# Optimization experiments

Measured on AMD Instinct MI355X. Metric: run time of the kernel, lower is better.

The kernel has to match this reference:

```python
import jax, jax.numpy as jnp
import numpy as np

N_EMBD = 256; N_HEAD = 16; CTX = 2048
V_HD = 32; KV_RANK = 32; Q_RANK = 96
ROPE_HD = 64; NOPE_HD = 32; HEAD_D = ROPE_HD + NOPE_HD  # 96
N_KEEP = CTX // 4  # 512
C_CURV = 1.0
EPS = 1e-6
B, T = 2, 2048


def rmsnorm(x, w):
    return x * jax.lax.rsqrt(jnp.mean(x * x, axis=-1, keepdims=True) + EPS) * w


def logmap(x, u, c):
    # log map from hyperbolic point x toward u (Poincare ball, curvature c)
    xn = jnp.linalg.norm(x, axis=-1, keepdims=True)
    sf = 2.0 / (1.0 + c * xn ** 2)                      # scaling_factor(x, c)
    mx = -x
    un = jnp.linalg.norm(u, axis=-1, keepdims=True)
    ip = jnp.sum(mx * u, axis=-1, keepdims=True)
    num = (1 + 2 * c * ip + c * un ** 2) * mx + (1 - c * xn ** 2) * u
    den = 1 + 2 * c * ip + (c ** 2) * (xn ** 2) * (un ** 2)
    mob = num / den                                      # mobius_addition(-x, u, c)
    an = jnp.linalg.norm(mob, axis=-1, keepdims=True)
    cf = 2.0 / (sf * (c ** 0.5))
    arg = jnp.clip(jnp.sqrt(c) * jnp.sqrt(an), -0.999, 0.999)
    return cf * jnp.arctanh(arg) * (mob / an)


def rope_apply(x, cos_seq, sin_seq):
    # x: [B,H,T,D]; cos/sin: [T,D//2] -> broadcast [1,1,T,D//2]
    c = cos_seq[None, None]; s = sin_seq[None, None]
    xr, xi = jnp.split(x, 2, axis=-1)
    return jnp.concatenate([xr * c - xi * s, xr * s + xi * c], axis=-1)


def attn(q, k, v, causal):
    d = q.shape[-1]
    s = jnp.einsum('bhqd,bhkd->bhqk', q, k) / jnp.sqrt(jnp.asarray(d, q.dtype))
    if causal:
        mask = jnp.tril(jnp.ones((s.shape[-2], s.shape[-1]), bool))
        s = jnp.where(mask, s, -jnp.inf)
    p = jax.nn.softmax(s, axis=-1)
    return jnp.einsum('bhqk,bhkd->bhqd', p, v)


def setup_inputs() -> dict:
    key = jax.random.key(0)
    ks = jax.random.split(key, 20)
    w = lambda k, shp: (jax.random.normal(k, shp, jnp.float32) * 0.02)
    NOPE_DIM = N_HEAD * NOPE_HD   # 512
    ROPE_DIM = N_HEAD * ROPE_HD   # 1024
    VAL_DIM = N_HEAD * V_HD       # 512
    # precompute_freqs_cis(rope_head_dim, ctx_len)
    freqs = 1.0 / (10000.0 ** (np.arange(0, ROPE_HD, 2, dtype=np.float32) / ROPE_HD))
    t = np.arange(CTX, dtype=np.float32)
    ang = np.outer(t, freqs)
    return {
        'x': jax.random.normal(ks[0], (B, T, N_EMBD), jnp.float32),
        'W_cq': w(ks[1], (N_EMBD, Q_RANK)),
        'q_norm_w': jnp.ones((Q_RANK,), jnp.float32),
        'W_dqn': w(ks[2], (Q_RANK, NOPE_DIM)),
        'W_dqr': w(ks[3], (Q_RANK, ROPE_DIM)),
        'W_ckv': w(ks[4], (N_EMBD, KV_RANK)),
        'kv_norm_w': jnp.ones((KV_RANK,), jnp.float32),
        'W_dkn': w(ks[5], (KV_RANK, NOPE_DIM)),
        'W_dv': w(ks[6], (KV_RANK, VAL_DIM)),
        'W_kr': w(ks[7], (N_EMBD, ROPE_HD)),
        'W_imp': w(ks[8], (N_EMBD, 1)),
        'b_imp': jnp.zeros((1,), jnp.float32),
        'W_selk': w(ks[9], (N_EMBD, N_HEAD * HEAD_D)),
        'W_selv': w(ks[10], (N_EMBD, VAL_DIM)),
        'W_wink': w(ks[11], (N_EMBD, N_HEAD * HEAD_D)),
        'W_winv': w(ks[12], (N_EMBD, VAL_DIM)),
        'W_gate': w(ks[13], (N_EMBD, 3)),
        'b_gate': jnp.zeros((3,), jnp.float32),
        'W_proj': w(ks[14], (N_HEAD * V_HD, N_EMBD)),
        'cos_f': jnp.asarray(np.cos(ang)),
        'sin_f': jnp.asarray(np.sin(ang)),
    }


def reference(x, W_cq, q_norm_w, W_dqn, W_dqr, W_ckv, kv_norm_w, W_dkn, W_dv, W_kr,
              W_imp, b_imp, W_selk, W_selv, W_wink, W_winv, W_gate, b_gate, W_proj,
              cos_f, sin_f):
    Bx, Tx, C = x.shape
    ref = jnp.pad(x[:, :-1, :], ((0, 0), (1, 0), (0, 0)))   # calculate_reference_point
    xh = logmap(ref, x, C_CURV)
    # compressed query path
    nq = rmsnorm(xh @ W_cq, q_norm_w)
    qn = (nq @ W_dqn).reshape(Bx, Tx, N_HEAD, NOPE_HD).transpose(0, 2, 1, 3)
    qr = (nq @ W_dqr).reshape(Bx, Tx, N_HEAD, ROPE_HD).transpose(0, 2, 1, 3)
    qr = rope_apply(qr, cos_f[:Tx], sin_f[:Tx])
    q = jnp.concatenate([qn, qr], axis=-1)                  # [B,H,T,96]
    # branch gate
    bw = jax.nn.softmax(jnp.mean(x @ W_gate + b_gate, axis=1), axis=-1)  # [B,3]
    # compressed KV path
    nkv = rmsnorm(x @ W_ckv, kv_norm_w)
    kn = (nkv @ W_dkn).reshape(Bx, Tx, N_HEAD, NOPE_HD).transpose(0, 2, 1, 3)
    v = (nkv @ W_dv).reshape(Bx, Tx, N_HEAD, V_HD).transpose(0, 2, 1, 3)
    kr = rope_apply((x @ W_kr)[:, None], cos_f[:Tx], sin_f[:Tx])  # [B,1,T,64]
    kr = jnp.broadcast_to(kr, (Bx, N_HEAD, Tx, ROPE_HD))
    k = jnp.concatenate([kn, kr], axis=-1)
    out_cmp = attn(q, k, v, causal=True)
    # token-selection branch (top-k important tokens, sorted)
    scores = (x @ W_imp + b_imp)[..., 0]                    # [B,T]
    _, idx = jax.lax.top_k(scores, min(N_KEEP, Tx))
    idx = jnp.sort(idx, axis=1)
    sel = jnp.take_along_axis(x, idx[:, :, None], axis=1)   # [B,K,C]
    sk = (sel @ W_selk).reshape(Bx, -1, N_HEAD, HEAD_D).transpose(0, 2, 1, 3)
    sv = (sel @ W_selv).reshape(Bx, -1, N_HEAD, V_HD).transpose(0, 2, 1, 3)
    out_sel = attn(q, sk, sv, causal=False)
    # sliding-window branch (training path -> full sequence, causal)
    wk = (x @ W_wink).reshape(Bx, Tx, N_HEAD, HEAD_D).transpose(0, 2, 1, 3)
    wv = (x @ W_winv).reshape(Bx, Tx, N_HEAD, V_HD).transpose(0, 2, 1, 3)
    out_win = attn(q, wk, wv, causal=True)
    w3 = bw[:, :, None, None, None]
    out = w3[:, 0] * out_cmp + w3[:, 1] * out_sel + w3[:, 2] * out_win
    out = out.transpose(0, 2, 1, 3).reshape(Bx, Tx, N_HEAD * V_HD)
    return out @ W_proj
```

## Files before the change

### kernel.cpp

```cpp
#include <hip/hip_runtime.h>
#include <hip/hip_bf16.h>
#include <math.h>

#define TT 2048
#define NE 256
#define NHEAD 16

typedef __attribute__((ext_vector_type(8))) short bf16x8;
typedef __attribute__((ext_vector_type(4))) float f32x4;
typedef __attribute__((ext_vector_type(16))) float f32x16;
typedef unsigned short ushort;
typedef __attribute__((ext_vector_type(8))) unsigned short us8;

__device__ __forceinline__ short f2bf(float x) {
  __hip_bfloat16 h = __float2bfloat16(x);
  return *reinterpret_cast<short*>(&h);
}
__device__ __forceinline__ float bf2f(ushort u) {
  unsigned v = ((unsigned)u) << 16;
  return __uint_as_float(v);
}

__global__ __launch_bounds__(256) void prep_kernel(
    const float* __restrict__ x, ushort* __restrict__ xhb, ushort* __restrict__ xbf,
    const float* __restrict__ W_dqn, const float* __restrict__ W_dqr,
    const float* __restrict__ W_dkn, const float* __restrict__ W_dv,
    const float* __restrict__ W_selk, const float* __restrict__ W_selv,
    const float* __restrict__ W_wink, const float* __restrict__ W_winv,
    const float* __restrict__ W_proj, const float* __restrict__ W_cq,
    const float* __restrict__ W_ckv, const float* __restrict__ W_kr,
    const float* __restrict__ W_gate, const float* __restrict__ W_imp,
    ushort* __restrict__ Wt_q, ushort* __restrict__ Wt_kv,
    ushort* __restrict__ Wt_sel, ushort* __restrict__ Wt_win,
    ushort* __restrict__ Wt_proj, ushort* __restrict__ Wt_cq,
    ushort* __restrict__ Wt_nkv, float* __restrict__ gacc) {
  __shared__ float red[16];
  int bx = blockIdx.x, tid = threadIdx.x;
  if (bx < 4096) {
    int row = bx;
    int t = row & (TT - 1);
    float uv = x[row * NE + tid];
    float rv = (t == 0) ? 0.f : x[row * NE - NE + tid];
    xbf[row * NE + tid] = (ushort)f2bf(uv);
    float a = rv * rv, bq = uv * uv, c2 = -rv * uv;
#pragma unroll
    for (int off = 32; off > 0; off >>= 1) {
      a += __shfl_down(a, off, 64);
      bq += __shfl_down(bq, off, 64);
      c2 += __shfl_down(c2, off, 64);
    }
    if ((tid & 63) == 0) {
      int w = tid >> 6;
      red[w] = a; red[4 + w] = bq; red[8 + w] = c2;
    }
    __syncthreads();
    float xn2 = red[0] + red[1] + red[2] + red[3];
    float un2 = red[4] + red[5] + red[6] + red[7];
    float ip  = red[8] + red[9] + red[10] + red[11];
    float den = 1.f + 2.f * ip + xn2 * un2;
    float mob = ((1.f + 2.f * ip + un2) * (-rv) + (1.f - xn2) * uv) / den;
    float m2 = mob * mob;
#pragma unroll
    for (int off = 32; off > 0; off >>= 1) m2 += __shfl_down(m2, off, 64);
    if ((tid & 63) == 0) red[12 + (tid >> 6)] = m2;
    __syncthreads();
    float an2 = red[12] + red[13] + red[14] + red[15];
    float an = sqrtf(an2);
    float cf = 1.f + xn2;
    float arg = fminf(sqrtf(an), 0.999f);
    xhb[row * NE + tid] = (ushort)f2bf(cf * atanhf(arg) * mob / an);
    return;
  }
  int i = (bx - 4096) * 256 + tid;
  const float scale = 0.147244458176154f;
  if (i < 147456) {
    int k = i / 1536, n = i - k * 1536;
    float v = (n < 512) ? W_dqn[(size_t)k * 512 + n] : W_dqr[(size_t)k * 1024 + (n - 512)];
    Wt_q[(size_t)n * 96 + k] = (ushort)f2bf(v * scale);
  } else if (i < 180224) {
    int j = i - 147456;
    int k = j >> 10, n = j & 1023;
    float v = (n < 512) ? W_dkn[(size_t)k * 512 + n] : W_dv[(size_t)k * 512 + (n - 512)];
    Wt_kv[(size_t)n * 32 + k] = (ushort)f2bf(v);
  } else if (i < 704512) {
    int j = i - 180224;
    int k = j >> 11, n = j & 2047;
    float v = (n < 1536) ? W_selk[(size_t)k * 1536 + n] : W_selv[(size_t)k * 512 + (n - 1536)];
    Wt_sel[(size_t)n * 256 + k] = (ushort)f2bf(v);
  } else if (i < 1228800) {
    int j = i - 704512;
    int k = j >> 11, n = j & 2047;
    float v = (n < 1536) ? W_wink[(size_t)k * 1536 + n] : W_winv[(size_t)k * 512 + (n - 1536)];
    Wt_win[(size_t)n * 256 + k] = (ushort)f2bf(v);
  } else if (i < 1359872) {
    int j = i - 1228800;
    int k = j >> 8, n = j & 255;
    Wt_proj[(size_t)n * 512 + k] = (ushort)f2bf(W_proj[(size_t)k * 256 + n]);
  } else if (i < 1392640) {
    int j = i - 1359872;
    int k = j >> 7, n = j & 127;
    float v = (n < 96) ? W_cq[(size_t)k * 96 + n] : 0.f;
    Wt_cq[(size_t)n * 256 + k] = (ushort)f2bf(v);
  } else if (i < 1425408) {
    int j = i - 1392640;
    int k = j >> 7, n = j & 127;
    float v;
    if (n < 32) v = W_ckv[(size_t)k * 32 + n];
    else if (n < 96) v = W_kr[(size_t)k * 64 + (n - 32)];
    else if (n < 99) v = W_gate[(size_t)k * 3 + (n - 96)];
    else if (n == 99) v = W_imp[k];
    else v = 0.f;
    Wt_nkv[(size_t)n * 256 + k] = (ushort)f2bf(v);
  } else if (i < 1425414) {
    gacc[i - 1425408] = 0.f;
  }
}

__global__ __launch_bounds__(256) void gemm_kernel(const ushort* __restrict__ A,
                                                   const ushort* __restrict__ Bt,
                                                   void* __restrict__ Out,
                                                   const ushort* __restrict__ A2,
                                                   const ushort* __restrict__ Bt2,
                                                   void* __restrict__ Out2,
                                                   const int* __restrict__ selidx2,
                                                   const float* __restrict__ cosp,
                                                   const float* __restrict__ sinp,
                                                   float* __restrict__ gateacc,
                                                   const float* __restrict__ kvnw,
                                                   const float* __restrict__ qnw,
                                                   const float* __restrict__ bimp,
                                                   ushort* __restrict__ krbf_o,
                                                   float* __restrict__ scores_o,
                                                   int fusenorm,
                                                   int K, int ldo, int obf16, int ropemode,
                                                   int K2, int ldo2, int obf2, int rope2,
                                                   int xlim2, int ylim2) {
  __shared__ __align__(16) short gsm[2 * 128 * 40];
  short* As = gsm;
  short* Bs = gsm + 128 * 40;
  const int* selidx = nullptr;
  if (blockIdx.z == 1) {
    if ((int)blockIdx.x >= xlim2 || (int)blockIdx.y >= ylim2) return;
    A = A2; Bt = Bt2; Out = Out2; selidx = selidx2;
    K = K2; ldo = ldo2; obf16 = obf2; ropemode = rope2;
  }
  int m0 = blockIdx.x * 128, n0 = blockIdx.y * 128;
  int tid = threadIdx.x;
  int wv = tid >> 6, lane = tid & 63;
  int l15 = lane & 15, quad = lane >> 4;
  int wm = wv >> 1, wn = wv & 1;

  int r = tid >> 1, seg = tid & 1;
  int arow = m0 + r;
  if (selidx) arow = ((arow >> 9) * TT) + selidx[m0 + r];
  const ushort* ga = A + (size_t)arow * K + seg * 16;
  const ushort* gb = Bt + (size_t)(n0 + r) * K + seg * 16;

  f32x4 acc[4][4];
#pragma unroll
  for (int i = 0; i < 4; ++i)
#pragma unroll
    for (int j = 0; j < 4; ++j) acc[i][j] = (f32x4){0.f, 0.f, 0.f, 0.f};

  int nk = K >> 5;
  us8 apre0 = *(const us8*)ga, apre1 = *(const us8*)(ga + 8);
  us8 bpre0 = *(const us8*)gb, bpre1 = *(const us8*)(gb + 8);
  for (int kk = 0; kk < nk; ++kk) {
    __syncthreads();
    *(us8*)(As + r * 40 + seg * 16) = apre0;
    *(us8*)(As + r * 40 + seg * 16 + 8) = apre1;
    *(us8*)(Bs + r * 40 + seg * 16) = bpre0;
    *(us8*)(Bs + r * 40 + seg * 16 + 8) = bpre1;
    __syncthreads();
    if (kk + 1 < nk) {
      apre0 = *(const us8*)(ga + (kk + 1) * 32);
      apre1 = *(const us8*)(ga + (kk + 1) * 32 + 8);
      bpre0 = *(const us8*)(gb + (kk + 1) * 32);
      bpre1 = *(const us8*)(gb + (kk + 1) * 32 + 8);
    }
    bf16x8 af[4], bf[4];
#pragma unroll
    for (int mf = 0; mf < 4; ++mf)
      af[mf] = *(const bf16x8*)(As + (wm * 64 + mf * 16 + l15) * 40 + quad * 8);
#pragma unroll
    for (int nf = 0; nf < 4; ++nf)
      bf[nf] = *(const bf16x8*)(Bs + (wn * 64 + nf * 16 + l15) * 40 + quad * 8);
#pragma unroll
    for (int mf = 0; mf < 4; ++mf)
#pragma unroll
      for (int nf = 0; nf < 4; ++nf)
        acc[mf][nf] = __builtin_amdgcn_mfma_f32_16x16x32_bf16(af[mf], bf[nf], acc[mf][nf], 0, 0, 0);
  }

  if (fusenorm) {
    __syncthreads();
    float* sc = (float*)gsm;
    if (blockIdx.z == 0) {
      float ss[4][4];
#pragma unroll
      for (int mf = 0; mf < 4; ++mf)
#pragma unroll
        for (int reg = 0; reg < 4; ++reg) {
          float p = acc[mf][0][reg] * acc[mf][0][reg] + acc[mf][1][reg] * acc[mf][1][reg];
          if (wn == 0) p += acc[mf][2][reg] * acc[mf][2][reg] + acc[mf][3][reg] * acc[mf][3][reg];
#pragma unroll
          for (int off = 8; off > 0; off >>= 1) p += __shfl_xor(p, off, 64);
          ss[mf][reg] = p;
        }
      if (l15 == 0) {
#pragma unroll
        for (int mf = 0; mf < 4; ++mf)
#pragma unroll
          for (int reg = 0; reg < 4; ++reg)
            sc[wn * 128 + wm * 64 + mf * 16 + quad * 4 + reg] = ss[mf][reg];
      }
      __syncthreads();
#pragma unroll
      for (int mf = 0; mf < 4; ++mf) {
#pragma unroll
        for (int nf = 0; nf < 4; ++nf) {
          if (wn == 1 && nf >= 2) continue;
          int col = wn * 64 + nf * 16 + l15;
#pragma unroll
          for (int reg = 0; reg < 4; ++reg) {
            int rl = wm * 64 + mf * 16 + quad * 4 + reg;
            float sstot = sc[rl] + sc[128 + rl];
            float sca = rsqrtf(sstot / 96.f + 1e-6f) * qnw[col];
            ((ushort*)Out)[(size_t)(m0 + rl) * 96 + col] = (ushort)f2bf(acc[mf][nf][reg] * sca);
          }
        }
      }
    } else {
      if (wn == 1 && l15 < 3) {
        float g = 0.f;
#pragma unroll
        for (int mf = 0; mf < 4; ++mf)
#pragma unroll
          for (int reg = 0; reg < 4; ++reg) g += acc[mf][2][reg];
        atomicAdd(&gateacc[(m0 >> 11) * 3 + l15], g);
      }
      if (wn == 1 && l15 == 3) {
#pragma unroll
        for (int mf = 0; mf < 4; ++mf)
#pragma unroll
          for (int reg = 0; reg < 4; ++reg)
            scores_o[m0 + wm * 64 + mf * 16 + quad * 4 + reg] = acc[mf][2][reg] + bimp[0];
      }
      if (wn == 0) {
#pragma unroll
        for (int mf = 0; mf < 4; ++mf) {
          float ssr[4];
#pragma unroll
          for (int reg = 0; reg < 4; ++reg) {
            float p = acc[mf][0][reg] * acc[mf][0][reg] + acc[mf][1][reg] * acc[mf][1][reg];
#pragma unroll
            for (int off = 8; off > 0; off >>= 1) p += __shfl_xor(p, off, 64);
            ssr[reg] = p;
          }
#pragma unroll
          for (int nf = 0; nf < 2; ++nf) {
            int col = nf * 16 + l15;
#pragma unroll
            for (int reg = 0; reg < 4; ++reg) {
              int rl = wm * 64 + mf * 16 + quad * 4 + reg;
              float sca = rsqrtf(ssr[reg] / 32.f + 1e-6f) * kvnw[col];
              ((ushort*)Out)[(size_t)(m0 + rl) * 32 + col] = (ushort)f2bf(acc[mf][nf][reg] * sca);
            }
          }
        }
      }
      if (wn == 1) {
#pragma unroll
        for (int mf = 0; mf < 4; ++mf)
#pragma unroll
          for (int nf = 0; nf < 2; ++nf) {
            int dd = nf * 16 + l15;
#pragma unroll
            for (int reg = 0; reg < 4; ++reg) {
              int rl = wm * 64 + mf * 16 + quad * 4 + reg;
              sc[rl * 33 + dd] = acc[mf][nf][reg];
            }
          }
      }
      __syncthreads();
      if (wn == 0) {
#pragma unroll
        for (int mf = 0; mf < 4; ++mf)
#pragma unroll
          for (int nf = 2; nf < 4; ++nf) {
            int dd = (nf - 2) * 16 + l15;
#pragma unroll
            for (int reg = 0; reg < 4; ++reg) {
              int rl = wm * 64 + mf * 16 + quad * 4 + reg;
              int grow = m0 + rl;
              int t = grow & (TT - 1);
              float c = cosp[t * 32 + dd], s = sinp[t * 32 + dd];
              float xr = acc[mf][nf][reg], xi = sc[rl * 33 + dd];
              krbf_o[(size_t)grow * 64 + dd] = (ushort)f2bf(xr * c - xi * s);
              krbf_o[(size_t)grow * 64 + dd + 32] = (ushort)f2bf(xr * s + xi * c);
            }
          }
      }
    }
    return;
  }

  if (ropemode && blockIdx.y >= 4) {
#pragma unroll
    for (int mf = 0; mf < 4; ++mf) {
#pragma unroll
      for (int nf = 0; nf < 2; ++nf) {
        int dd = nf * 16 + l15;
#pragma unroll
        for (int reg = 0; reg < 4; ++reg) {
          int row = m0 + wm * 64 + mf * 16 + quad * 4 + reg;
          int t = row & (TT - 1);
          float c = cosp[t * 32 + dd], s = sinp[t * 32 + dd];
          float xr = acc[mf][nf][reg], xi = acc[mf][nf + 2][reg];
          int col = n0 + wn * 64 + nf * 16 + l15;
          size_t oi = (size_t)row * ldo + col;
          ((ushort*)Out)[oi] = (ushort)f2bf(xr * c - xi * s);
          ((ushort*)Out)[oi + 32] = (ushort)f2bf(xr * s + xi * c);
        }
      }
    }
    return;
  }
#pragma unroll
  for (int mf = 0; mf < 4; ++mf) {
#pragma unroll
    for (int nf = 0; nf < 4; ++nf) {
#pragma unroll
      for (int reg = 0; reg < 4; ++reg) {
        int row = m0 + wm * 64 + mf * 16 + quad * 4 + reg;
        int col = n0 + wn * 64 + nf * 16 + l15;
        size_t oi = (size_t)row * ldo + col;
        float v = acc[mf][nf][reg];
        if (obf16) ((ushort*)Out)[oi] = (ushort)f2bf(v);
        else ((float*)Out)[oi] = v;
      }
    }
  }
}

__global__ __launch_bounds__(1024) void topk_rank_kernel(const float* __restrict__ scores,
                                                         int* __restrict__ flags) {
  int b = blockIdx.y, blk = blockIdx.x;
  int tid = threadIdx.x;
  __shared__ unsigned sk[TT];
#pragma unroll
  for (int e = 0; e < 2; ++e) {
    int i = tid + e * 1024;
    float s = scores[b * TT + i];
    unsigned u = __float_as_uint(s);
    u = (u & 0x80000000u) ? ~u : (u | 0x80000000u);
    sk[i] = u;
  }
  __syncthreads();
  int e = blk * 64 + (tid >> 4);
  int sub = tid & 15;
  unsigned u = sk[e];
  int r = 0;
  int j0 = sub * 128;
#pragma unroll 8
  for (int j = j0; j < j0 + 128; ++j) {
    unsigned v = sk[j];
    r += (int)((v > u) || (v == u && j < e));
  }
#pragma unroll
  for (int off = 8; off > 0; off >>= 1) r += __shfl_down(r, off, 16);
  if (sub == 0) flags[b * TT + e] = (r < 512) ? 1 : 0;
}

__global__ __launch_bounds__(1024) void topk_scan_kernel(const int* __restrict__ flags,
                                                         int* __restrict__ selidx) {
  int b = blockIdx.x, tid = threadIdx.x;
  __shared__ int wsum[16];
  int2 f = *(const int2*)(flags + b * TT + 2 * tid);
  int local = f.x + f.y;
  int lane = tid & 63, wv = tid >> 6;
  int sc = local;
#pragma unroll
  for (int off = 1; off < 64; off <<= 1) {
    int t = __shfl_up(sc, off, 64);
    if (lane >= off) sc += t;
  }
  if (lane == 63) wsum[wv] = sc;
  __syncthreads();
  int woff = 0;
  for (int w = 0; w < wv; ++w) woff += wsum[w];
  int p0 = woff + (sc - local) + f.x;
  int p1 = p0 + f.y;
  if (f.x) selidx[b * 512 + p0 - 1] = 2 * tid;
  if (f.y) selidx[b * 512 + p1 - 1] = 2 * tid + 1;
}

__global__ __launch_bounds__(512, 4) void flash_fused_kernel(
    const ushort* __restrict__ qbf,
    const ushort* __restrict__ kv,
    const ushort* __restrict__ krbf,
    const ushort* __restrict__ selt,
    const ushort* __restrict__ wint,
    const float* __restrict__ gacc,
    const float* __restrict__ b_gate,
    ushort* __restrict__ attout) {
  __shared__ __align__(16) short smem[13312 + 13312 + 4608 + 256];
  short* Qsm = smem;
  short* Ksm = smem + 13312;
  short* Vtm = smem + 26624;
  float* Ls  = (float*)(smem + 31232);

  int bx = blockIdx.x;
  int j = bx >> 5;
  int qtile = (j < 8) ? (15 - 2 * j) : (2 * (j - 8));
  int bh = bx & 31;
  int b = bh >> 4, h = bh & 15;
  int tid = threadIdx.x;
  int wv = tid >> 6;
  int qsub = wv >> 1;
  int khalf = wv & 1;
  int lane = tid & 63;
  int l31 = lane & 31, half = lane >> 5;

  float w0, w1, w2;
  {
    float g0 = gacc[b * 3 + 0] * (1.0f / 2048.0f) + b_gate[0];
    float g1 = gacc[b * 3 + 1] * (1.0f / 2048.0f) + b_gate[1];
    float g2 = gacc[b * 3 + 2] * (1.0f / 2048.0f) + b_gate[2];
    float mx = fmaxf(g0, fmaxf(g1, g2));
    float e0 = expf(g0 - mx), e1 = expf(g1 - mx), e2 = expf(g2 - mx);
    float inv = 1.f / (e0 + e1 + e2);
    w0 = e0 * inv; w1 = e1 * inv; w2 = e2 * inv;
  }

  int qrow0 = qtile * 128;
  for (int i = tid; i < 128 * 24; i += 512) {
    int qi = i / 24, dp = (i - qi * 24) * 4;
    int col = (dp < 32) ? (h * 32 + dp) : (512 + h * 64 + (dp - 32));
    *(ushort4*)(Qsm + qi * 104 + dp) =
        *(const ushort4*)(qbf + (size_t)(b * TT + qrow0 + qi) * 1536 + col);
  }

  short* kdst[3];
#pragma unroll
  for (int c = 0; c < 3; ++c) {
    int i = c * 512 + tid;
    int kj = i / 24, dp = (i - kj * 24) * 4;
    kdst[c] = &Ksm[kj * 104 + dp];
  }
  int vd0 = (tid & 15) * 2, vkjp = (tid >> 4) * 2;
  short* vdsta = &Vtm[(vd0 + 0) * 72 + vkjp];
  short* vdstb = &Vtm[(vd0 + 1) * 72 + vkjp];

  f32x16 oacc;
#pragma unroll
  for (int r2 = 0; r2 < 16; ++r2) oacc[r2] = 0.f;

#define PREFETCH(KP, VA, VB)                                  \
  {                                                           \
    _Pragma("unroll") for (int c = 0; c < 3; ++c) {           \
      KP[c] = *(const ushort4*)ksrc[c];                       \
      ksrc[c] += kstep[c];                                    \
    }                                                         \
    VA = *(const ushort2*)vsrcA;                              \
    VB = *(const ushort2*)vsrcB;                              \
    vsrcA += vstep;                                           \
    vsrcB += vstep;                                           \
  }

#define COMMIT(KP, VA, VB, SL)                                           \
  {                                                                      \
    _Pragma("unroll") for (int c = 0; c < 3; ++c)                        \
      *(ushort4*)(kdst[c] + (SL) * (64 * 104)) = KP[c];                  \
    *(unsigned*)(vdsta + (SL) * (32 * 72)) =                             \
        (unsigned)VA.x | ((unsigned)VB.x << 16);                         \
    *(unsigned*)(vdstb + (SL) * (32 * 72)) =                             \
        (unsigned)VA.y | ((unsigned)VB.y << 16);                         \
  }

  for (int s = 0; s < 3; ++s) {
    const ushort *kb1, *kb2, *vb;
    size_t krs1, krs2, vrs;
    int split, Tk, causal;
    if (s == 0) {
      kb1 = kv + h * 32;        krs1 = 1024; split = 32;
      kb2 = krbf;               krs2 = 64;
      vb = kv + 512 + h * 32;   vrs = 1024;
      Tk = TT; causal = 1;
    } else if (s == 1) {
      kb1 = selt + h * 96;      krs1 = 2048; split = 96;
      kb2 = selt;               krs2 = 2048;
      vb = selt + 1536 + h * 32; vrs = 2048;
      Tk = 512; causal = 0;
    } else {
      kb1 = wint + h * 96;      krs1 = 2048; split = 96;
      kb2 = wint;               krs2 = 2048;
      vb = wint + 1536 + h * 32; vrs = 2048;
      Tk = TT; causal = 1;
    }
    size_t bTk = (size_t)b * Tk;

    const ushort* ksrc[3];
    int kstep[3];
#pragma unroll
    for (int c = 0; c < 3; ++c) {
      int i = c * 512 + tid;
      int kj = i / 24, dp = (i - kj * 24) * 4;
      if (dp < split) { ksrc[c] = kb1 + (bTk + kj) * krs1 + dp; kstep[c] = (int)(64 * krs1); }
      else            { ksrc[c] = kb2 + (bTk + kj) * krs2 + (dp - split); kstep[c] = (int)(64 * krs2); }
    }
    const ushort* vsrcA = vb + (bTk + vkjp) * vrs + vd0;
    const ushort* vsrcB = vb + (bTk + vkjp + 1) * vrs + vd0;
    int vstep = (int)(64 * vrs);

    ushort4 kpre0[3], kpre1[3];
    ushort2 vpa0, vpb0, vpa1, vpb1;

    f32x16 of;
#pragma unroll
    for (int r2 = 0; r2 < 16; ++r2) of[r2] = 0.f;
    float lsum = 0.f;

    auto do_tile = [&](int kt, const short* Kss, const short* Vss) {
      int krow0 = kt * 64;
      const short* Qrow = Qsm + (qsub * 32 + l31) * 104 + half * 8;
      f32x16 sfT[2];
#pragma unroll
      for (int r2 = 0; r2 < 16; ++r2) { sfT[0][r2] = 0.f; sfT[1][r2] = 0.f; }
#pragma unroll
      for (int ks = 0; ks < 6; ++ks) {
        bf16x8 qk = *(const bf16x8*)(Qrow + ks * 16);
#pragma unroll
        for (int kb = 0; kb < 2; ++kb) {
          bf16x8 ak = *(const bf16x8*)(Kss + (kb * 32 + l31) * 104 + ks * 16 + half * 8);
          sfT[kb] = __builtin_amdgcn_mfma_f32_32x32x16_bf16(ak, qk, sfT[kb], 0, 0, 0);
        }
      }
      int qg = qrow0 + qsub * 32 + l31;
      int domask = causal && (kt >= 2 * qtile);
      unsigned w01[2][4], w23[2][4];
#pragma unroll
      for (int kb = 0; kb < 2; ++kb) {
#pragma unroll
        for (int gg = 0; gg < 4; ++gg) {
          int key0 = krow0 + kb * 32 + 8 * gg + 4 * half;
          float t0 = sfT[kb][gg * 4 + 0];
          float t1 = sfT[kb][gg * 4 + 1];
          float t2 = sfT[kb][gg * 4 + 2];
          float t3 = sfT[kb][gg * 4 + 3];
          if (domask) {
            if (key0 + 0 > qg) t0 = -INFINITY;
            if (key0 + 1 > qg) t1 = -INFINITY;
            if (key0 + 2 > qg) t2 = -INFINITY;
            if (key0 + 3 > qg) t3 = -INFINITY;
          }
          float p0 = __builtin_amdgcn_exp2f(fminf(t0, 43.3f));
          float p1 = __builtin_amdgcn_exp2f(fminf(t1, 43.3f));
          float p2 = __builtin_amdgcn_exp2f(fminf(t2, 43.3f));
          float p3 = __builtin_amdgcn_exp2f(fminf(t3, 43.3f));
          lsum += (p0 + p1) + (p2 + p3);
          asm("v_cvt_pk_bf16_f32 %0, %1, %2" : "=v"(w01[kb][gg]) : "v"(p0), "v"(p1));
          asm("v_cvt_pk_bf16_f32 %0, %1, %2" : "=v"(w23[kb][gg]) : "v"(p2), "v"(p3));
        }
      }
#pragma unroll
      for (int ks2 = 0; ks2 < 4; ++ks2) {
        int kb = ks2 >> 1, gA = 2 * (ks2 & 1);
        unsigned a0 = w01[kb][gA], b0 = w01[kb][gA + 1];
        unsigned a1 = w23[kb][gA], b1 = w23[kb][gA + 1];
        asm("v_permlane32_swap_b32 %0, %1" : "+v"(a0), "+v"(b0));
        asm("v_permlane32_swap_b32 %0, %1" : "+v"(a1), "+v"(b1));
        union { unsigned u[4]; bf16x8 v; } ap;
        ap.u[0] = a0; ap.u[1] = a1; ap.u[2] = b0; ap.u[3] = b1;
        bf16x8 bv = *(const bf16x8*)(Vss + l31 * 72 + ks2 * 16 + half * 8);
        of = __builtin_amdgcn_mfma_f32_32x32x16_bf16(ap.v, bv, of, 0, 0, 0);
      }
    };

    int nkt = causal ? (2 * qtile + 2) : 8;
    PREFETCH(kpre0, vpa0, vpb0);
    PREFETCH(kpre1, vpa1, vpb1);
    for (int kt = 0; kt < nkt; kt += 2) {
      __syncthreads();
      COMMIT(kpre0, vpa0, vpb0, 0);
      COMMIT(kpre1, vpa1, vpb1, 1);
      if (kt + 2 < nkt) PREFETCH(kpre0, vpa0, vpb0);
      if (kt + 3 < nkt) PREFETCH(kpre1, vpa1, vpb1);
      __syncthreads();
      if (khalf == 0) do_tile(kt, Ksm, Vtm);
      else            do_tile(kt + 1, Ksm + 64 * 104, Vtm + 32 * 72);
    }

    lsum += __shfl_xor(lsum, 32, 64);
    __syncthreads();
    float* red = (float*)Ksm;
    int rbase = (qsub * 64 + lane) * 17;
    if (khalf == 1) {
#pragma unroll
      for (int r2 = 0; r2 < 16; ++r2) red[rbase + r2] = of[r2];
      red[rbase + 16] = lsum;
    }
    __syncthreads();
    if (khalf == 0) {
#pragma unroll
      for (int r2 = 0; r2 < 16; ++r2) of[r2] += red[rbase + r2];
      lsum += red[rbase + 16];
      if (half == 0) Ls[qsub * 32 + l31] = lsum;
    }
    asm volatile("s_waitcnt lgkmcnt(0)" ::: "memory");
    if (khalf == 0) {
      float wgt = (s == 0) ? w0 : ((s == 1) ? w1 : w2);
#pragma unroll
      for (int reg = 0; reg < 16; ++reg) {
        int ql = (reg & 3) + 8 * (reg >> 2) + 4 * half;
        oacc[reg] += of[reg] * (wgt / Ls[qsub * 32 + ql]);
      }
    }
  }
#undef PREFETCH
#undef COMMIT

  if (khalf == 0) {
#pragma unroll
    for (int reg = 0; reg < 16; ++reg) {
      int trow = qrow0 + qsub * 32 + (reg & 3) + 8 * (reg >> 2) + 4 * half;
      attout[(size_t)(b * TT + trow) * 512 + h * 32 + l31] = (ushort)f2bf(oacc[reg]);
    }
  }
}

extern "C" void kernel_launch(void* const* d_in, const int* in_sizes, int n_in,
                              void* d_out, int out_size, void* d_ws, size_t ws_size,
                              hipStream_t stream) {
  const float* x      = (const float*)d_in[0];
  const float* W_cq   = (const float*)d_in[1];
  const float* qnw    = (const float*)d_in[2];
  const float* W_dqn  = (const float*)d_in[3];
  const float* W_dqr  = (const float*)d_in[4];
  const float* W_ckv  = (const float*)d_in[5];
  const float* kvnw   = (const float*)d_in[6];
  const float* W_dkn  = (const float*)d_in[7];
  const float* W_dv   = (const float*)d_in[8];
  const float* W_kr   = (const float*)d_in[9];
  const float* W_imp  = (const float*)d_in[10];
  const float* b_imp  = (const float*)d_in[11];
  const float* W_selk = (const float*)d_in[12];
  const float* W_selv = (const float*)d_in[13];
  const float* W_wink = (const float*)d_in[14];
  const float* W_winv = (const float*)d_in[15];
  const float* W_gate = (const float*)d_in[16];
  const float* b_gate = (const float*)d_in[17];
  const float* W_proj = (const float*)d_in[18];
  const float* cos_f  = (const float*)d_in[19];
  const float* sin_f  = (const float*)d_in[20];
  float* out = (float*)d_out;
  float* ws  = (float*)d_ws;

  size_t off = 0;
  auto alloc = [&](size_t n) {
    float* p = ws + off;
    off += (n + 255) & ~(size_t)255;
    return p;
  };
  const int ROWS = 2 * TT;
  ushort* xbf     = (ushort*)alloc((size_t)ROWS * 128);
  ushort* xhb     = (ushort*)alloc((size_t)ROWS * 128);
  ushort* nqb     = (ushort*)alloc((size_t)ROWS * 48);
  ushort* qbf     = (ushort*)alloc((size_t)ROWS * 768);
  ushort* nkvb    = (ushort*)alloc((size_t)ROWS * 16);
  ushort* kvtmp   = (ushort*)alloc((size_t)ROWS * 512);
  ushort* krbf    = (ushort*)alloc((size_t)ROWS * 32);
  float* scores   = alloc(ROWS);
  float* gacc     = alloc(8);
  int* selidx     = (int*)alloc(1024);
  int* selflags   = (int*)alloc(ROWS);
  ushort* seltmp  = (ushort*)alloc((size_t)1024 * 1024);
  ushort* wintmp  = (ushort*)alloc((size_t)ROWS * 1024);
  ushort* attoutb = (ushort*)alloc((size_t)ROWS * 256);
  ushort* Wt_q    = (ushort*)alloc((size_t)1536 * 48);
  ushort* Wt_kv   = (ushort*)alloc((size_t)1024 * 16);
  ushort* Wt_sel  = (ushort*)alloc((size_t)2048 * 128);
  ushort* Wt_win  = (ushort*)alloc((size_t)2048 * 128);
  ushort* Wt_proj = (ushort*)alloc((size_t)256 * 256);
  ushort* Wt_cq   = (ushort*)alloc((size_t)128 * 128);
  ushort* Wt_nkv  = (ushort*)alloc((size_t)128 * 128);

  prep_kernel<<<4096 + 5569, 256, 0, stream>>>(
      x, xhb, xbf,
      W_dqn, W_dqr, W_dkn, W_dv, W_selk, W_selv, W_wink, W_winv, W_proj,
      W_cq, W_ckv, W_kr, W_gate, W_imp,
      Wt_q, Wt_kv, Wt_sel, Wt_win, Wt_proj, Wt_cq, Wt_nkv, gacc);

  gemm_kernel<<<dim3(32, 1, 2), 256, 0, stream>>>(
      xhb, Wt_cq, nqb, xbf, Wt_nkv, nkvb,
      nullptr, cos_f, sin_f, gacc,
      kvnw, qnw, b_imp, krbf, scores, 1,
      256, 96, 1, 0, 256, 32, 1, 0, 32, 1);

  gemm_kernel<<<dim3(32, 12, 2), 256, 0, stream>>>(
      nqb, Wt_q, qbf, nkvb, Wt_kv, kvtmp,
      nullptr, cos_f, sin_f, nullptr,
      nullptr, nullptr, nullptr, nullptr, nullptr, 0,
      96, 1536, 1, 1, 32, 1024, 1, 0, 32, 8);

  topk_rank_kernel<<<dim3(32, 2), 1024, 0, stream>>>(scores, selflags);
  topk_scan_kernel<<<2, 1024, 0, stream>>>(selflags, selidx);

  gemm_kernel<<<dim3(32, 16, 2), 256, 0, stream>>>(
      xbf, Wt_win, wintmp, xbf, Wt_sel, seltmp,
      selidx, nullptr, nullptr, nullptr,
      nullptr, nullptr, nullptr, nullptr, nullptr, 0,
      256, 2048, 1, 0, 256, 2048, 1, 0, 8, 16);

  flash_fused_kernel<<<512, 512, 0, stream>>>(qbf, kvtmp, krbf, seltmp, wintmp,
                                              gacc, b_gate, attoutb);

  gemm_kernel<<<dim3(32, 2, 1), 256, 0, stream>>>(
      attoutb, Wt_proj, out, nullptr, nullptr, nullptr,
      nullptr, nullptr, nullptr, nullptr,
      nullptr, nullptr, nullptr, nullptr, nullptr, 0,
      512, 256, 0, 0, 0, 0, 0, 0, 0, 0);
}
```

Before: 274.4 us.

## Tile weight transposes through LDS and interleave QK/PV per key block

The weight-conversion part of the prep kernel now transposes 64x64 tiles through shared memory, so both the fp32 reads and the bf16 writes are coalesced. This replaces the old per-element scatter, which made strided writes and needed about 5.5k blocks; only 368 blocks are now launched. The attention inner tile is also restructured to compute scores, softmax and the PV MFMA one 32-key block at a time, which lowers register pressure from holding two score accumulators. The larger static LDS allocation in the prep kernel also applies to the row blocks and could reduce their occupancy.

```diff
diff --git a/kernel.cpp b/kernel.cpp
--- a/kernel.cpp
+++ b/kernel.cpp
@@ -35,6 +35,7 @@
     ushort* __restrict__ Wt_proj, ushort* __restrict__ Wt_cq,
     ushort* __restrict__ Wt_nkv, float* __restrict__ gacc) {
   __shared__ float red[16];
+  __shared__ float tl[64 * 65];
   int bx = blockIdx.x, tid = threadIdx.x;
   if (bx < 4096) {
     int row = bx;
@@ -71,48 +72,67 @@
     xhb[row * NE + tid] = (ushort)f2bf(cf * atanhf(arg) * mob / an);
     return;
   }
-  int i = (bx - 4096) * 256 + tid;
-  const float scale = 0.147244458176154f;
-  if (i < 147456) {
-    int k = i / 1536, n = i - k * 1536;
-    float v = (n < 512) ? W_dqn[(size_t)k * 512 + n] : W_dqr[(size_t)k * 1024 + (n - 512)];
-    Wt_q[(size_t)n * 96 + k] = (ushort)f2bf(v * scale);
-  } else if (i < 180224) {
-    int j = i - 147456;
-    int k = j >> 10, n = j & 1023;
-    float v = (n < 512) ? W_dkn[(size_t)k * 512 + n] : W_dv[(size_t)k * 512 + (n - 512)];
-    Wt_kv[(size_t)n * 32 + k] = (ushort)f2bf(v);
-  } else if (i < 704512) {
-    int j = i - 180224;
-    int k = j >> 11, n = j & 2047;
-    float v = (n < 1536) ? W_selk[(size_t)k * 1536 + n] : W_selv[(size_t)k * 512 + (n - 1536)];
-    Wt_sel[(size_t)n * 256 + k] = (ushort)f2bf(v);
-  } else if (i < 1228800) {
-    int j = i - 704512;
-    int k = j >> 11, n = j & 2047;
-    float v = (n < 1536) ? W_wink[(size_t)k * 1536 + n] : W_winv[(size_t)k * 512 + (n - 1536)];
-    Wt_win[(size_t)n * 256 + k] = (ushort)f2bf(v);
-  } else if (i < 1359872) {
-    int j = i - 1228800;
-    int k = j >> 8, n = j & 255;
-    Wt_proj[(size_t)n * 512 + k] = (ushort)f2bf(W_proj[(size_t)k * 256 + n]);
-  } else if (i < 1392640) {
-    int j = i - 1359872;
-    int k = j >> 7, n = j & 127;
-    float v = (n < 96) ? W_cq[(size_t)k * 96 + n] : 0.f;
-    Wt_cq[(size_t)n * 256 + k] = (ushort)f2bf(v);
-  } else if (i < 1425408) {
-    int j = i - 1392640;
-    int k = j >> 7, n = j & 127;
-    float v;
-    if (n < 32) v = W_ckv[(size_t)k * 32 + n];
-    else if (n < 96) v = W_kr[(size_t)k * 64 + (n - 32)];
-    else if (n < 99) v = W_gate[(size_t)k * 3 + (n - 96)];
-    else if (n == 99) v = W_imp[k];
-    else v = 0.f;
-    Wt_nkv[(size_t)n * 256 + k] = (ushort)f2bf(v);
-  } else if (i < 1425414) {
-    gacc[i - 1425408] = 0.f;
+  int tix = bx - 4096;
+  if (tix == 0 && tid < 6) gacc[tid] = 0.f;
+  int which, tn, tk, N, K;
+  ushort* D;
+  float scl = 1.f;
+  if (tix < 48) {
+    which = 0; tn = tix >> 1; tk = tix & 1; N = 1536; K = 96; D = Wt_q;
+    scl = 0.147244458176154f;
+  } else if (tix < 64) {
+    which = 1; tn = tix - 48; tk = 0; N = 1024; K = 32; D = Wt_kv;
+  } else if (tix < 192) {
+    which = 2; int idx = tix - 64; tn = idx >> 2; tk = idx & 3; N = 2048; K = 256; D = Wt_sel;
+  } else if (tix < 320) {
+    which = 3; int idx = tix - 192; tn = idx >> 2; tk = idx & 3; N = 2048; K = 256; D = Wt_win;
+  } else if (tix < 352) {
+    which = 4; int idx = tix - 320; tn = idx >> 3; tk = idx & 7; N = 256; K = 512; D = Wt_proj;
+  } else if (tix < 360) {
+    which = 5; int idx = tix - 352; tn = idx >> 2; tk = idx & 3; N = 128; K = 256; D = Wt_cq;
+  } else {
+    which = 6; int idx = tix - 360; tn = idx >> 2; tk = idx & 3; N = 128; K = 256; D = Wt_nkv;
+  }
+  int n0 = tn * 64, k0 = tk * 64;
+#pragma unroll
+  for (int it = 0; it < 16; ++it) {
+    int flat = it * 256 + tid;
+    int kk = flat >> 6, nn = flat & 63;
+    int k = k0 + kk, n = n0 + nn;
+    float v = 0.f;
+    if (k < K) {
+      if (which == 0)      v = ((n < 512) ? W_dqn[(size_t)k * 512 + n]
+                                          : W_dqr[(size_t)k * 1024 + (n - 512)]) * scl;
+      else if (which == 1) v = (n < 512) ? W_dkn[(size_t)k * 512 + n]
+                                         : W_dv[(size_t)k * 512 + (n - 512)];
+      else if (which == 2) v = (n < 1536) ? W_selk[(size_t)k * 1536 + n]
+                                          : W_selv[(size_t)k * 512 + (n - 1536)];
+      else if (which == 3) v = (n < 1536) ? W_wink[(size_t)k * 1536 + n]
+                                          : W_winv[(size_t)k * 512 + (n - 1536)];
+      else if (which == 4) v = W_proj[(size_t)k * 256 + n];
+      else if (which == 5) v = (n < 96) ? W_cq[(size_t)k * 96 + n] : 0.f;
+      else {
+        if (n < 32)       v = W_ckv[(size_t)k * 32 + n];
+        else if (n < 96)  v = W_kr[(size_t)k * 64 + (n - 32)];
+        else if (n < 99)  v = W_gate[(size_t)k * 3 + (n - 96)];
+        else if (n == 99) v = W_imp[k];
+      }
+    }
+    tl[kk * 65 + nn] = v;
+  }
+  __syncthreads();
+#pragma unroll
+  for (int it = 0; it < 4; ++it) {
+    int flat = it * 256 + tid;
+    int nl = flat >> 4, k4 = (flat & 15) * 4;
+    if (k0 + k4 < K) {
+      ushort4 o;
+      o.x = (ushort)f2bf(tl[(k4 + 0) * 65 + nl]);
+      o.y = (ushort)f2bf(tl[(k4 + 1) * 65 + nl]);
+      o.z = (ushort)f2bf(tl[(k4 + 2) * 65 + nl]);
+      o.w = (ushort)f2bf(tl[(k4 + 3) * 65 + nl]);
+      *(ushort4*)(D + (size_t)(n0 + nl) * K + k0 + k4) = o;
+    }
   }
 }
 
@@ -524,30 +544,27 @@
     auto do_tile = [&](int kt, const short* Kss, const short* Vss) {
       int krow0 = kt * 64;
       const short* Qrow = Qsm + (qsub * 32 + l31) * 104 + half * 8;
-      f32x16 sfT[2];
-#pragma unroll
-      for (int r2 = 0; r2 < 16; ++r2) { sfT[0][r2] = 0.f; sfT[1][r2] = 0.f; }
-#pragma unroll
-      for (int ks = 0; ks < 6; ++ks) {
-        bf16x8 qk = *(const bf16x8*)(Qrow + ks * 16);
-#pragma unroll
-        for (int kb = 0; kb < 2; ++kb) {
-          bf16x8 ak = *(const bf16x8*)(Kss + (kb * 32 + l31) * 104 + ks * 16 + half * 8);
-          sfT[kb] = __builtin_amdgcn_mfma_f32_32x32x16_bf16(ak, qk, sfT[kb], 0, 0, 0);
-        }
-      }
       int qg = qrow0 + qsub * 32 + l31;
       int domask = causal && (kt >= 2 * qtile);
-      unsigned w01[2][4], w23[2][4];
 #pragma unroll
       for (int kb = 0; kb < 2; ++kb) {
+        f32x16 sfT;
+#pragma unroll
+        for (int r2 = 0; r2 < 16; ++r2) sfT[r2] = 0.f;
+#pragma unroll
+        for (int ks = 0; ks < 6; ++ks) {
+          bf16x8 qk = *(const bf16x8*)(Qrow + ks * 16);
+          bf16x8 ak = *(const bf16x8*)(Kss + (kb * 32 + l31) * 104 + ks * 16 + half * 8);
+          sfT = __builtin_amdgcn_mfma_f32_32x32x16_bf16(ak, qk, sfT, 0, 0, 0);
+        }
+        unsigned w01[4], w23[4];
 #pragma unroll
         for (int gg = 0; gg < 4; ++gg) {
           int key0 = krow0 + kb * 32 + 8 * gg + 4 * half;
-          float t0 = sfT[kb][gg * 4 + 0];
-          float t1 = sfT[kb][gg * 4 + 1];
-          float t2 = sfT[kb][gg * 4 + 2];
-          float t3 = sfT[kb][gg * 4 + 3];
+          float t0 = sfT[gg * 4 + 0];
+          float t1 = sfT[gg * 4 + 1];
+          float t2 = sfT[gg * 4 + 2];
+          float t3 = sfT[gg * 4 + 3];
           if (domask) {
             if (key0 + 0 > qg) t0 = -INFINITY;
             if (key0 + 1 > qg) t1 = -INFINITY;
@@ -559,21 +576,21 @@
           float p2 = __builtin_amdgcn_exp2f(fminf(t2, 43.3f));
           float p3 = __builtin_amdgcn_exp2f(fminf(t3, 43.3f));
           lsum += (p0 + p1) + (p2 + p3);
-          asm("v_cvt_pk_bf16_f32 %0, %1, %2" : "=v"(w01[kb][gg]) : "v"(p0), "v"(p1));
-          asm("v_cvt_pk_bf16_f32 %0, %1, %2" : "=v"(w23[kb][gg]) : "v"(p2), "v"(p3));
+          asm("v_cvt_pk_bf16_f32 %0, %1, %2" : "=v"(w01[gg]) : "v"(p0), "v"(p1));
+          asm("v_cvt_pk_bf16_f32 %0, %1, %2" : "=v"(w23[gg]) : "v"(p2), "v"(p3));
         }
-      }
-#pragma unroll
-      for (int ks2 = 0; ks2 < 4; ++ks2) {
-        int kb = ks2 >> 1, gA = 2 * (ks2 & 1);
-        unsigned a0 = w01[kb][gA], b0 = w01[kb][gA + 1];
-        unsigned a1 = w23[kb][gA], b1 = w23[kb][gA + 1];
-        asm("v_permlane32_swap_b32 %0, %1" : "+v"(a0), "+v"(b0));
-        asm("v_permlane32_swap_b32 %0, %1" : "+v"(a1), "+v"(b1));
-        union { unsigned u[4]; bf16x8 v; } ap;
-        ap.u[0] = a0; ap.u[1] = a1; ap.u[2] = b0; ap.u[3] = b1;
-        bf16x8 bv = *(const bf16x8*)(Vss + l31 * 72 + ks2 * 16 + half * 8);
-        of = __builtin_amdgcn_mfma_f32_32x32x16_bf16(ap.v, bv, of, 0, 0, 0);
+#pragma unroll
+        for (int k2 = 0; k2 < 2; ++k2) {
+          int gA = 2 * k2;
+          unsigned a0 = w01[gA], b0 = w01[gA + 1];
+          unsigned a1 = w23[gA], b1 = w23[gA + 1];
+          asm("v_permlane32_swap_b32 %0, %1" : "+v"(a0), "+v"(b0));
+          asm("v_permlane32_swap_b32 %0, %1" : "+v"(a1), "+v"(b1));
+          union { unsigned u[4]; bf16x8 v; } ap;
+          ap.u[0] = a0; ap.u[1] = a1; ap.u[2] = b0; ap.u[3] = b1;
+          bf16x8 bv = *(const bf16x8*)(Vss + l31 * 72 + (kb * 2 + k2) * 16 + half * 8);
+          of = __builtin_amdgcn_mfma_f32_32x32x16_bf16(ap.v, bv, of, 0, 0, 0);
+        }
       }
     };
 
@@ -685,7 +702,7 @@
   ushort* Wt_cq   = (ushort*)alloc((size_t)128 * 128);
   ushort* Wt_nkv  = (ushort*)alloc((size_t)128 * 128);
 
-  prep_kernel<<<4096 + 5569, 256, 0, stream>>>(
+  prep_kernel<<<4096 + 368, 256, 0, stream>>>(
       x, xhb, xbf,
       W_dqn, W_dqr, W_dkn, W_dv, W_selk, W_selv, W_wink, W_winv, W_proj,
       W_cq, W_ckv, W_kr, W_gate, W_imp,
```

New measurement: 281.1 us. 2.4% more time.
